# Kernel tuning notes

Measured on AMD Instinct MI355X. Metric: run time of the kernel, lower is better.

Reference implementation:

```python
import jax, jax.numpy as jnp
import numpy as np

B, N, C, W = 8, 2048, 256, 256

def setup_inputs() -> dict:
    key = jax.random.key(0)
    ks = jax.random.split(key, 8)
    x = jax.random.normal(ks[0], (B, N, C), dtype=jnp.float32)
    valid_len = jax.random.randint(ks[1], (B,), 0, N)
    # kaiming_normal_ on weights (fan_in = C), default bias init ~ U(-1/sqrt(C), 1/sqrt(C))
    std = np.sqrt(2.0 / C).astype(np.float32)
    bb = 1.0 / np.sqrt(C)
    Wq = jax.random.normal(ks[2], (W, C), dtype=jnp.float32) * std
    Wk = jax.random.normal(ks[3], (W, C), dtype=jnp.float32) * std
    Wv = jax.random.normal(ks[4], (W, C), dtype=jnp.float32) * std
    bq = jax.random.uniform(ks[5], (W,), dtype=jnp.float32, minval=-bb, maxval=bb)
    bk = jax.random.uniform(ks[6], (W,), dtype=jnp.float32, minval=-bb, maxval=bb)
    bv = jax.random.uniform(ks[7], (W,), dtype=jnp.float32, minval=-bb, maxval=bb)
    return {"x": x, "Wq": Wq, "bq": bq, "Wk": Wk, "bk": bk, "Wv": Wv, "bv": bv, "valid_len": valid_len}

def reference(x, Wq, bq, Wk, bk, Wv, bv, valid_len):
    # valid_len is unused in the original forward
    q = jax.nn.relu(jnp.einsum('bnc,wc->bnw', x, Wq) + bq)  # [B,N,W]
    k = jax.nn.relu(jnp.einsum('bnc,wc->bnw', x, Wk) + bk)
    v = jax.nn.relu(jnp.einsum('bnc,wc->bnw', x, Wv) + bv)
    scores = jnp.einsum('biw,bjw->bij', q, k) / jnp.sqrt(jnp.float32(k.shape[1]))  # [B,N,N]
    attn = jax.nn.softmax(scores, axis=1)  # NOTE: softmax over the QUERY axis (dim=1), as in source
    out = jnp.einsum('bij,bjw->biw', attn, v)
    return out + q
```

## Files before the change

kernel.cpp:

```cpp
#include <hip/hip_runtime.h>
#include <math.h>

#define Bb 8
#define Nn 2048
#define Cc 256
#define Ww 256
#define Mtot (Bb*Nn)

typedef __attribute__((ext_vector_type(8))) short bf16x8;
typedef __attribute__((ext_vector_type(4))) float f32x4;

__device__ __forceinline__ ushort bf16_rne(float f) {
    uint u = __float_as_uint(f);
    return (ushort)((u + 0x7FFFu + ((u >> 16) & 1u)) >> 16);
}
__device__ __forceinline__ float bf16_to_f32(ushort h) {
    return __uint_as_float(((uint)h) << 16);
}

__global__ __launch_bounds__(256) void prep_kernel(
    const float* __restrict__ x,
    const float* __restrict__ Wq, const float* __restrict__ Wk,
    const float* __restrict__ Wv,
    ushort* __restrict__ xh, ushort* __restrict__ xl,
    ushort* __restrict__ wqh, ushort* __restrict__ wql,
    ushort* __restrict__ wkh, ushort* __restrict__ wkl,
    ushort* __restrict__ wvh, ushort* __restrict__ wvl)
{
    const int tid = threadIdx.x;
    const float* src;
    ushort *dh, *dl;
    size_t off;
    if (blockIdx.x < 4096) {
        off = ((size_t)blockIdx.x * 256 + tid) * 4;
        src = x; dh = xh; dl = xl;
    } else {
        size_t s = ((size_t)(blockIdx.x - 4096) * 256 + tid) * 4;
        int which = (int)(s >> 16);
        off = s & 65535u;
        src = (which == 0) ? Wq : ((which == 1) ? Wk : Wv);
        dh  = (which == 0) ? wqh : ((which == 1) ? wkh : wvh);
        dl  = (which == 0) ? wql : ((which == 1) ? wkl : wvl);
    }
    float4 v = *(const float4*)(src + off);
    ushort4 h, l;
    h.x = bf16_rne(v.x); l.x = bf16_rne(v.x - bf16_to_f32(h.x));
    h.y = bf16_rne(v.y); l.y = bf16_rne(v.y - bf16_to_f32(h.y));
    h.z = bf16_rne(v.z); l.z = bf16_rne(v.z - bf16_to_f32(h.z));
    h.w = bf16_rne(v.w); l.w = bf16_rne(v.w - bf16_to_f32(h.w));
    *(ushort4*)(dh + off) = h;
    *(ushort4*)(dl + off) = l;
}

__global__ __launch_bounds__(256) void qkv_mfma_kernel(
    const ushort* __restrict__ xh, const ushort* __restrict__ xl,
    const ushort* __restrict__ wqh, const ushort* __restrict__ wql,
    const ushort* __restrict__ wkh, const ushort* __restrict__ wkl,
    const ushort* __restrict__ wvh, const ushort* __restrict__ wvl,
    const float* __restrict__ bq, const float* __restrict__ bk,
    const float* __restrict__ bv,
    float* __restrict__ v32,
    ushort* __restrict__ qhi, ushort* __restrict__ qlo,
    ushort* __restrict__ khi, ushort* __restrict__ klo)
{
    __shared__ ushort lah[4096], lal[4096], lbh[4096], lbl[4096];

    const int tid = threadIdx.x;
    const int m0 = blockIdx.x * 128;
    const int yy = blockIdx.y;
    const int which = yy >> 1;
    const int w0 = (yy & 1) * 128;

    const ushort* wh_ = (which == 0) ? wqh : ((which == 1) ? wkh : wvh);
    const ushort* wl_ = (which == 0) ? wql : ((which == 1) ? wkl : wvl);
    const float*  bm  = (which == 0) ? bq  : ((which == 1) ? bk  : bv);

    const ushort* ah_ = xh + (size_t)m0 * Cc;
    const ushort* al_ = xl + (size_t)m0 * Cc;
    const ushort* bh_ = wh_ + (size_t)w0 * Cc;
    const ushort* bl_ = wl_ + (size_t)w0 * Cc;

    const int wave = tid >> 6, lane = tid & 63;
    const int wy = wave >> 1, wx = wave & 1;
    const int lrow = lane & 15, lg = lane >> 4;

    f32x4 acc[4][4];
    #pragma unroll
    for (int a = 0; a < 4; ++a)
        #pragma unroll
        for (int c = 0; c < 4; ++c) acc[a][c] = (f32x4){0.f, 0.f, 0.f, 0.f};

    const int cg = tid & 3;
    const int cr0 = tid >> 2;

    for (int kc = 0; kc < Cc; kc += 32) {
        #pragma unroll
        for (int h = 0; h < 2; ++h) {
            int r = cr0 + h * 64;
            int gg = cg ^ ((r >> 1) & 3);
            int li = r * 32 + gg * 8;
            size_t go = (size_t)r * Cc + kc + cg * 8;
            *(bf16x8*)&lah[li] = *(const bf16x8*)(ah_ + go);
            *(bf16x8*)&lal[li] = *(const bf16x8*)(al_ + go);
            *(bf16x8*)&lbh[li] = *(const bf16x8*)(bh_ + go);
            *(bf16x8*)&lbl[li] = *(const bf16x8*)(bl_ + go);
        }
        __syncthreads();

        bf16x8 ah[4], al[4], bh[4], bl[4];
        #pragma unroll
        for (int t = 0; t < 4; ++t) {
            int ra = wy * 64 + t * 16 + lrow;
            int ia = ra * 32 + ((lg ^ ((ra >> 1) & 3)) * 8);
            ah[t] = *(const bf16x8*)&lah[ia];
            al[t] = *(const bf16x8*)&lal[ia];
            int rb = wx * 64 + t * 16 + lrow;
            int ib = rb * 32 + ((lg ^ ((rb >> 1) & 3)) * 8);
            bh[t] = *(const bf16x8*)&lbh[ib];
            bl[t] = *(const bf16x8*)&lbl[ib];
        }
        #pragma unroll
        for (int jt = 0; jt < 4; ++jt)
            #pragma unroll
            for (int it = 0; it < 4; ++it) {
                acc[jt][it] = __builtin_amdgcn_mfma_f32_16x16x32_bf16(ah[jt], bh[it], acc[jt][it], 0, 0, 0);
                acc[jt][it] = __builtin_amdgcn_mfma_f32_16x16x32_bf16(ah[jt], bl[it], acc[jt][it], 0, 0, 0);
                acc[jt][it] = __builtin_amdgcn_mfma_f32_16x16x32_bf16(al[jt], bh[it], acc[jt][it], 0, 0, 0);
            }
        __syncthreads();
    }

    ushort* hp = (which == 0) ? qhi : khi;
    ushort* lp = (which == 0) ? qlo : klo;
    #pragma unroll
    for (int it = 0; it < 4; ++it) {
        const int w = w0 + wx * 64 + it * 16 + lrow;
        const float bias = bm[w];
        #pragma unroll
        for (int jt = 0; jt < 4; ++jt) {
            const int mb = m0 + wy * 64 + jt * 16 + lg * 4;
            #pragma unroll
            for (int rg = 0; rg < 4; ++rg) {
                float val = fmaxf(acc[jt][it][rg] + bias, 0.f);
                size_t o = (size_t)(mb + rg) * Ww + w;
                if (which == 2) {
                    v32[o] = val;
                } else {
                    ushort h = bf16_rne(val);
                    hp[o] = h;
                    lp[o] = bf16_rne(val - bf16_to_f32(h));
                }
            }
        }
    }
}

__global__ __launch_bounds__(256) void scores_mfma_kernel(
    const ushort* __restrict__ qhi, const ushort* __restrict__ qlo,
    const ushort* __restrict__ khi, const ushort* __restrict__ klo,
    ushort* __restrict__ eh, float* __restrict__ dpart)
{
    __shared__ ushort lkh[4096], lkl[4096], lqh[4096], lql[4096];

    const int tid = threadIdx.x;
    const int i0 = blockIdx.x * 128;
    const int j0 = blockIdx.y * 128;
    const int b  = blockIdx.z;

    const ushort* kh = khi + ((size_t)b * Nn + j0) * Ww;
    const ushort* kl = klo + ((size_t)b * Nn + j0) * Ww;
    const ushort* qh = qhi + ((size_t)b * Nn + i0) * Ww;
    const ushort* ql = qlo + ((size_t)b * Nn + i0) * Ww;

    const int wave = tid >> 6, lane = tid & 63;
    const int wy = wave >> 1, wx = wave & 1;
    const int lrow = lane & 15, lg = lane >> 4;

    f32x4 acc[4][4];
    #pragma unroll
    for (int a = 0; a < 4; ++a)
        #pragma unroll
        for (int c = 0; c < 4; ++c) acc[a][c] = (f32x4){0.f, 0.f, 0.f, 0.f};

    const int cg = tid & 3;
    const int cr0 = tid >> 2;

    for (int kc = 0; kc < Ww; kc += 32) {
        #pragma unroll
        for (int h = 0; h < 2; ++h) {
            int r = cr0 + h * 64;
            int gg = cg ^ ((r >> 1) & 3);
            int li = r * 32 + gg * 8;
            size_t go = (size_t)r * Ww + kc + cg * 8;
            *(bf16x8*)&lkh[li] = *(const bf16x8*)(kh + go);
            *(bf16x8*)&lkl[li] = *(const bf16x8*)(kl + go);
            *(bf16x8*)&lqh[li] = *(const bf16x8*)(qh + go);
            *(bf16x8*)&lql[li] = *(const bf16x8*)(ql + go);
        }
        __syncthreads();

        bf16x8 ah[4], al[4], bh[4], bl[4];
        #pragma unroll
        for (int t = 0; t < 4; ++t) {
            int ra = wy * 64 + t * 16 + lrow;
            int ia = ra * 32 + ((lg ^ ((ra >> 1) & 3)) * 8);
            ah[t] = *(const bf16x8*)&lkh[ia];
            al[t] = *(const bf16x8*)&lkl[ia];
            int rb = wx * 64 + t * 16 + lrow;
            int ib = rb * 32 + ((lg ^ ((rb >> 1) & 3)) * 8);
            bh[t] = *(const bf16x8*)&lqh[ib];
            bl[t] = *(const bf16x8*)&lql[ib];
        }
        #pragma unroll
        for (int jt = 0; jt < 4; ++jt)
            #pragma unroll
            for (int it = 0; it < 4; ++it) {
                acc[jt][it] = __builtin_amdgcn_mfma_f32_16x16x32_bf16(ah[jt], bh[it], acc[jt][it], 0, 0, 0);
                acc[jt][it] = __builtin_amdgcn_mfma_f32_16x16x32_bf16(ah[jt], bl[it], acc[jt][it], 0, 0, 0);
                acc[jt][it] = __builtin_amdgcn_mfma_f32_16x16x32_bf16(al[jt], bh[it], acc[jt][it], 0, 0, 0);
            }
        __syncthreads();
    }

    const float scale = 0.02209708691207961f;
    ushort* ehb = eh + (size_t)b * Nn * Nn;
    float* dpb  = dpart + (size_t)b * Nn;

    float esum[4][4];
    #pragma unroll
    for (int jt = 0; jt < 4; ++jt)
        #pragma unroll
        for (int rg = 0; rg < 4; ++rg) esum[jt][rg] = 0.f;

    #pragma unroll
    for (int jt = 0; jt < 4; ++jt) {
        const int jb = j0 + wy * 64 + jt * 16 + lg * 4;
        #pragma unroll
        for (int it = 0; it < 4; ++it) {
            const int i = i0 + wx * 64 + it * 16 + lrow;
            ushort4 h4;
            #pragma unroll
            for (int rg = 0; rg < 4; ++rg) {
                float e = __expf(acc[jt][it][rg] * scale);
                ushort hh = bf16_rne(e);
                (&h4.x)[rg] = hh;
                esum[jt][rg] += bf16_to_f32(hh);
            }
            *(ushort4*)(ehb + (size_t)i * Nn + jb) = h4;
        }
    }
    #pragma unroll
    for (int jt = 0; jt < 4; ++jt)
        #pragma unroll
        for (int rg = 0; rg < 4; ++rg) {
            float v = esum[jt][rg];
            v += __shfl_xor(v, 1);
            v += __shfl_xor(v, 2);
            v += __shfl_xor(v, 4);
            v += __shfl_xor(v, 8);
            if (lrow == 0)
                atomicAdd(dpb + j0 + wy * 64 + jt * 16 + lg * 4 + rg, v);
        }
}

__global__ __launch_bounds__(256) void vt_kernel(
    const float* __restrict__ v32, const float* __restrict__ dpart,
    ushort* __restrict__ vthi, ushort* __restrict__ vtlo)
{
    __shared__ ushort Thi[64*66], Tlo[64*66];
    const int tid = threadIdx.x;
    const int j0 = blockIdx.x * 64;
    const int w0 = blockIdx.y * 64;
    const int b  = blockIdx.z;
    const float* vb = v32 + (size_t)b * Nn * Ww;
    const float* dpb = dpart + (size_t)b * Nn;

    #pragma unroll
    for (int r = 0; r < 4; ++r) {
        int j  = (tid >> 4) + r * 16;
        int wl = (tid & 15) * 4;
        float invd = 1.0f / dpb[j0 + j];
        float4 tv = *(const float4*)(vb + (size_t)(j0 + j) * Ww + w0 + wl);
        float f[4] = {tv.x * invd, tv.y * invd, tv.z * invd, tv.w * invd};
        #pragma unroll
        for (int c = 0; c < 4; ++c) {
            ushort h = bf16_rne(f[c]);
            Thi[(wl + c) * 66 + j] = h;
            Tlo[(wl + c) * 66 + j] = bf16_rne(f[c] - bf16_to_f32(h));
        }
    }
    __syncthreads();
    {
        int wl = tid >> 2, jc = (tid & 3) * 16;
        size_t go = ((size_t)b * Ww + w0 + wl) * Nn + j0 + jc;
        uint tH[8], tL[8];
        #pragma unroll
        for (int u = 0; u < 8; ++u) {
            tH[u] = *(const uint*)&Thi[wl * 66 + jc + u * 2];
            tL[u] = *(const uint*)&Tlo[wl * 66 + jc + u * 2];
        }
        #pragma unroll
        for (int u = 0; u < 2; ++u) {
            uint4 hh; hh.x = tH[u*4+0]; hh.y = tH[u*4+1]; hh.z = tH[u*4+2]; hh.w = tH[u*4+3];
            uint4 ll; ll.x = tL[u*4+0]; ll.y = tL[u*4+1]; ll.z = tL[u*4+2]; ll.w = tL[u*4+3];
            *(uint4*)(vthi + go + u * 8) = hh;
            *(uint4*)(vtlo + go + u * 8) = ll;
        }
    }
}

__global__ __launch_bounds__(256) void pv_mfma_kernel(
    const ushort* __restrict__ eh,
    const ushort* __restrict__ vthi, const ushort* __restrict__ vtlo,
    float* __restrict__ part)
{
    __shared__ alignas(16) ushort Ah[128*40];
    __shared__ alignas(16) ushort Bh[64*40], Bl[64*40];

    const int tid = threadIdx.x;
    const int i0 = blockIdx.x * 128;
    const int wt = blockIdx.y & 3, kz = blockIdx.y >> 2;
    const int w0 = wt * 64;
    const int b  = blockIdx.z;

    const ushort* ehb = eh + (size_t)b * Nn * Nn;
    const ushort* vhb = vthi + (size_t)b * Ww * Nn;
    const ushort* vlb = vtlo + (size_t)b * Ww * Nn;

    const int wave = tid >> 6, lane = tid & 63;
    const int wy = wave >> 1, wx = wave & 1;
    const int lr = lane & 15, lg = lane >> 4;

    f32x4 acc[4][2];
    #pragma unroll
    for (int a = 0; a < 4; ++a)
        #pragma unroll
        for (int c = 0; c < 2; ++c) acc[a][c] = (f32x4){0.f, 0.f, 0.f, 0.f};

    const bool isA = tid < 128;
    const int srow = isA ? tid : (tid & 63);
    const ushort* gsrc = isA ? ehb : ((tid & 64) ? vlb : vhb);
    const size_t goff0 = isA
        ? ((size_t)(i0 + srow) * Nn + (size_t)kz * 1024)
        : ((size_t)(w0 + srow) * Nn + (size_t)kz * 1024);
    ushort* ldst = isA ? &Ah[srow * 40] : ((tid & 64) ? &Bl[srow * 40] : &Bh[srow * 40]);

    bf16x8 r0 = *(const bf16x8*)(gsrc + goff0);
    bf16x8 r1 = *(const bf16x8*)(gsrc + goff0 + 8);
    bf16x8 r2 = *(const bf16x8*)(gsrc + goff0 + 16);
    bf16x8 r3 = *(const bf16x8*)(gsrc + goff0 + 24);

    for (int ks = 0; ks < 32; ++ks) {
        *(bf16x8*)(ldst)      = r0;
        *(bf16x8*)(ldst + 8)  = r1;
        *(bf16x8*)(ldst + 16) = r2;
        *(bf16x8*)(ldst + 24) = r3;
        __syncthreads();

        if (ks < 31) {
            const size_t go = goff0 + (ks + 1) * 32;
            r0 = *(const bf16x8*)(gsrc + go);
            r1 = *(const bf16x8*)(gsrc + go + 8);
            r2 = *(const bf16x8*)(gsrc + go + 16);
            r3 = *(const bf16x8*)(gsrc + go + 24);
        }

        bf16x8 af[4], bfh[2], bfl[2];
        #pragma unroll
        for (int t = 0; t < 4; ++t)
            af[t] = *(const bf16x8*)&Ah[(wy * 64 + t * 16 + lr) * 40 + lg * 8];
        #pragma unroll
        for (int t = 0; t < 2; ++t) {
            const int br = (wx * 32 + t * 16 + lr) * 40 + lg * 8;
            bfh[t] = *(const bf16x8*)&Bh[br];
            bfl[t] = *(const bf16x8*)&Bl[br];
        }
        #pragma unroll
        for (int ia = 0; ia < 4; ++ia)
            #pragma unroll
            for (int ib = 0; ib < 2; ++ib) {
                acc[ia][ib] = __builtin_amdgcn_mfma_f32_16x16x32_bf16(af[ia], bfh[ib], acc[ia][ib], 0, 0, 0);
                acc[ia][ib] = __builtin_amdgcn_mfma_f32_16x16x32_bf16(af[ia], bfl[ib], acc[ia][ib], 0, 0, 0);
            }
        __syncthreads();
    }

    float* pout = part + (size_t)kz * Mtot * Ww;
    #pragma unroll
    for (int ia = 0; ia < 4; ++ia) {
        const int ibase = i0 + wy * 64 + ia * 16 + lg * 4;
        #pragma unroll
        for (int ib = 0; ib < 2; ++ib) {
            const int w = w0 + wx * 32 + ib * 16 + lr;
            #pragma unroll
            for (int rg = 0; rg < 4; ++rg)
                pout[((size_t)(b * Nn + ibase + rg)) * Ww + w] = acc[ia][ib][rg];
        }
    }
}

__global__ __launch_bounds__(256) void qadd_kernel(
    const float* __restrict__ part,
    const ushort* __restrict__ qhi, const ushort* __restrict__ qlo,
    float* __restrict__ out)
{
    const size_t g4 = ((size_t)blockIdx.x * 256 + threadIdx.x) * 4;
    float4 p0 = *(const float4*)(part + g4);
    float4 p1 = *(const float4*)(part + (size_t)Mtot * Ww + g4);
    ushort4 h = *(const ushort4*)(qhi + g4);
    ushort4 l = *(const ushort4*)(qlo + g4);
    float4 o;
    o.x = p0.x + p1.x + bf16_to_f32(h.x) + bf16_to_f32(l.x);
    o.y = p0.y + p1.y + bf16_to_f32(h.y) + bf16_to_f32(l.y);
    o.z = p0.z + p1.z + bf16_to_f32(h.z) + bf16_to_f32(l.z);
    o.w = p0.w + p1.w + bf16_to_f32(h.w) + bf16_to_f32(l.w);
    *(float4*)(out + g4) = o;
}

extern "C" void kernel_launch(void* const* d_in, const int* in_sizes, int n_in,
                              void* d_out, int out_size, void* d_ws, size_t ws_size,
                              hipStream_t stream) {
    const float* x  = (const float*)d_in[0];
    const float* Wq = (const float*)d_in[1];
    const float* bq = (const float*)d_in[2];
    const float* Wk = (const float*)d_in[3];
    const float* bk = (const float*)d_in[4];
    const float* Wv = (const float*)d_in[5];
    const float* bv = (const float*)d_in[6];
    float* out = (float*)d_out;

    float*  v32 = (float*)d_ws;
    ushort* qhi = (ushort*)(v32 + (size_t)Mtot * Ww);
    ushort* qlo = qhi + (size_t)Mtot * Ww;
    ushort* khi = qlo + (size_t)Mtot * Ww;
    ushort* klo = khi + (size_t)Mtot * Ww;
    ushort* eh  = klo + (size_t)Mtot * Ww;
    float*  part = (float*)(eh + (size_t)Bb * Nn * Nn);
    float*  dpart = part + (size_t)2 * Mtot * Ww;
    ushort* xh  = (ushort*)(dpart + Bb * Nn);
    ushort* xl  = xh + (size_t)Mtot * Cc;
    ushort* wqh = xl + (size_t)Mtot * Cc;
    ushort* wql = wqh + Ww * Cc;
    ushort* wkh = wql + Ww * Cc;
    ushort* wkl = wkh + Ww * Cc;
    ushort* wvh = wkl + Ww * Cc;
    ushort* wvl = wvh + Ww * Cc;
    ushort* vthi = khi;
    ushort* vtlo = klo;

    hipMemsetAsync(dpart, 0, (size_t)Bb * Nn * sizeof(float), stream);
    prep_kernel<<<dim3(4288), 256, 0, stream>>>(x, Wq, Wk, Wv, xh, xl,
                                                wqh, wql, wkh, wkl, wvh, wvl);
    qkv_mfma_kernel<<<dim3(128, 6), 256, 0, stream>>>(xh, xl, wqh, wql, wkh, wkl,
                                                      wvh, wvl, bq, bk, bv,
                                                      v32, qhi, qlo, khi, klo);
    scores_mfma_kernel<<<dim3(16, 16, 8), 256, 0, stream>>>(qhi, qlo, khi, klo, eh, dpart);
    vt_kernel<<<dim3(32, 4, 8), 256, 0, stream>>>(v32, dpart, vthi, vtlo);
    pv_mfma_kernel<<<dim3(16, 8, 8), 256, 0, stream>>>(eh, vthi, vtlo, part);
    qadd_kernel<<<dim3(4096), 256, 0, stream>>>(part, qhi, qlo, out);
}
```

Measured before the change: 286.3 us.

## Register-prefetch next K tile in QKV/scores GEMMs and widen PV tile

The QKV and scores GEMM kernels now load the next K chunk from global memory into registers while the current chunk is consumed from LDS, which hides global latency behind the MFMA work. Separately, the PV kernel tile grows from 128x64 to 128x128 over W, so each block reuses the loaded attention tile across twice as many output columns. The grid halves in y to match. This reduces redundant reads of the large exp-score matrix at the cost of more registers, more LDS and fewer blocks.

```diff
diff --git a/kernel.cpp b/kernel.cpp
--- a/kernel.cpp
+++ b/kernel.cpp
@@ -93,19 +93,41 @@
     const int cg = tid & 3;
     const int cr0 = tid >> 2;
 
+    bf16x8 sah[2], sal[2], sbh[2], sbl[2];
+    #pragma unroll
+    for (int h = 0; h < 2; ++h) {
+        int r = cr0 + h * 64;
+        size_t go = (size_t)r * Cc + cg * 8;
+        sah[h] = *(const bf16x8*)(ah_ + go);
+        sal[h] = *(const bf16x8*)(al_ + go);
+        sbh[h] = *(const bf16x8*)(bh_ + go);
+        sbl[h] = *(const bf16x8*)(bl_ + go);
+    }
+
     for (int kc = 0; kc < Cc; kc += 32) {
         #pragma unroll
         for (int h = 0; h < 2; ++h) {
             int r = cr0 + h * 64;
             int gg = cg ^ ((r >> 1) & 3);
             int li = r * 32 + gg * 8;
-            size_t go = (size_t)r * Cc + kc + cg * 8;
-            *(bf16x8*)&lah[li] = *(const bf16x8*)(ah_ + go);
-            *(bf16x8*)&lal[li] = *(const bf16x8*)(al_ + go);
-            *(bf16x8*)&lbh[li] = *(const bf16x8*)(bh_ + go);
-            *(bf16x8*)&lbl[li] = *(const bf16x8*)(bl_ + go);
+            *(bf16x8*)&lah[li] = sah[h];
+            *(bf16x8*)&lal[li] = sal[h];
+            *(bf16x8*)&lbh[li] = sbh[h];
+            *(bf16x8*)&lbl[li] = sbl[h];
         }
         __syncthreads();
+
+        if (kc + 32 < Cc) {
+            #pragma unroll
+            for (int h = 0; h < 2; ++h) {
+                int r = cr0 + h * 64;
+                size_t go = (size_t)r * Cc + kc + 32 + cg * 8;
+                sah[h] = *(const bf16x8*)(ah_ + go);
+                sal[h] = *(const bf16x8*)(al_ + go);
+                sbh[h] = *(const bf16x8*)(bh_ + go);
+                sbl[h] = *(const bf16x8*)(bl_ + go);
+            }
+        }
 
         bf16x8 ah[4], al[4], bh[4], bl[4];
         #pragma unroll
@@ -185,19 +207,41 @@
     const int cg = tid & 3;
     const int cr0 = tid >> 2;
 
+    bf16x8 skh[2], skl[2], sqh[2], sql[2];
+    #pragma unroll
+    for (int h = 0; h < 2; ++h) {
+        int r = cr0 + h * 64;
+        size_t go = (size_t)r * Ww + cg * 8;
+        skh[h] = *(const bf16x8*)(kh + go);
+        skl[h] = *(const bf16x8*)(kl + go);
+        sqh[h] = *(const bf16x8*)(qh + go);
+        sql[h] = *(const bf16x8*)(ql + go);
+    }
+
     for (int kc = 0; kc < Ww; kc += 32) {
         #pragma unroll
         for (int h = 0; h < 2; ++h) {
             int r = cr0 + h * 64;
             int gg = cg ^ ((r >> 1) & 3);
             int li = r * 32 + gg * 8;
-            size_t go = (size_t)r * Ww + kc + cg * 8;
-            *(bf16x8*)&lkh[li] = *(const bf16x8*)(kh + go);
-            *(bf16x8*)&lkl[li] = *(const bf16x8*)(kl + go);
-            *(bf16x8*)&lqh[li] = *(const bf16x8*)(qh + go);
-            *(bf16x8*)&lql[li] = *(const bf16x8*)(ql + go);
+            *(bf16x8*)&lkh[li] = skh[h];
+            *(bf16x8*)&lkl[li] = skl[h];
+            *(bf16x8*)&lqh[li] = sqh[h];
+            *(bf16x8*)&lql[li] = sql[h];
         }
         __syncthreads();
+
+        if (kc + 32 < Ww) {
+            #pragma unroll
+            for (int h = 0; h < 2; ++h) {
+                int r = cr0 + h * 64;
+                size_t go = (size_t)r * Ww + kc + 32 + cg * 8;
+                skh[h] = *(const bf16x8*)(kh + go);
+                skl[h] = *(const bf16x8*)(kl + go);
+                sqh[h] = *(const bf16x8*)(qh + go);
+                sql[h] = *(const bf16x8*)(ql + go);
+            }
+        }
 
         bf16x8 ah[4], al[4], bh[4], bl[4];
         #pragma unroll
@@ -315,12 +359,12 @@
     float* __restrict__ part)
 {
     __shared__ alignas(16) ushort Ah[128*40];
-    __shared__ alignas(16) ushort Bh[64*40], Bl[64*40];
+    __shared__ alignas(16) ushort Bh[128*40], Bl[128*40];
 
     const int tid = threadIdx.x;
     const int i0 = blockIdx.x * 128;
-    const int wt = blockIdx.y & 3, kz = blockIdx.y >> 2;
-    const int w0 = wt * 64;
+    const int wt = blockIdx.y & 1, kz = blockIdx.y >> 1;
+    const int w0 = wt * 128;
     const int b  = blockIdx.z;
 
     const ushort* ehb = eh + (size_t)b * Nn * Nn;
@@ -331,54 +375,57 @@
     const int wy = wave >> 1, wx = wave & 1;
     const int lr = lane & 15, lg = lane >> 4;
 
-    f32x4 acc[4][2];
+    f32x4 acc[4][4];
     #pragma unroll
     for (int a = 0; a < 4; ++a)
         #pragma unroll
-        for (int c = 0; c < 2; ++c) acc[a][c] = (f32x4){0.f, 0.f, 0.f, 0.f};
-
-    const bool isA = tid < 128;
-    const int srow = isA ? tid : (tid & 63);
-    const ushort* gsrc = isA ? ehb : ((tid & 64) ? vlb : vhb);
-    const size_t goff0 = isA
-        ? ((size_t)(i0 + srow) * Nn + (size_t)kz * 1024)
-        : ((size_t)(w0 + srow) * Nn + (size_t)kz * 1024);
-    ushort* ldst = isA ? &Ah[srow * 40] : ((tid & 64) ? &Bl[srow * 40] : &Bh[srow * 40]);
-
-    bf16x8 r0 = *(const bf16x8*)(gsrc + goff0);
-    bf16x8 r1 = *(const bf16x8*)(gsrc + goff0 + 8);
-    bf16x8 r2 = *(const bf16x8*)(gsrc + goff0 + 16);
-    bf16x8 r3 = *(const bf16x8*)(gsrc + goff0 + 24);
+        for (int c = 0; c < 4; ++c) acc[a][c] = (f32x4){0.f, 0.f, 0.f, 0.f};
+
+    const int srow = tid >> 1;
+    const int sjc  = (tid & 1) * 16;
+    const size_t aoff0 = (size_t)(i0 + srow) * Nn + (size_t)kz * 1024 + sjc;
+    const size_t boff0 = (size_t)(w0 + srow) * Nn + (size_t)kz * 1024 + sjc;
+    const int lbase = srow * 40 + sjc;
+
+    bf16x8 ra0 = *(const bf16x8*)(ehb + aoff0);
+    bf16x8 ra1 = *(const bf16x8*)(ehb + aoff0 + 8);
+    bf16x8 rh0 = *(const bf16x8*)(vhb + boff0);
+    bf16x8 rh1 = *(const bf16x8*)(vhb + boff0 + 8);
+    bf16x8 rl0 = *(const bf16x8*)(vlb + boff0);
+    bf16x8 rl1 = *(const bf16x8*)(vlb + boff0 + 8);
 
     for (int ks = 0; ks < 32; ++ks) {
-        *(bf16x8*)(ldst)      = r0;
-        *(bf16x8*)(ldst + 8)  = r1;
-        *(bf16x8*)(ldst + 16) = r2;
-        *(bf16x8*)(ldst + 24) = r3;
+        *(bf16x8*)&Ah[lbase]     = ra0;
+        *(bf16x8*)&Ah[lbase + 8] = ra1;
+        *(bf16x8*)&Bh[lbase]     = rh0;
+        *(bf16x8*)&Bh[lbase + 8] = rh1;
+        *(bf16x8*)&Bl[lbase]     = rl0;
+        *(bf16x8*)&Bl[lbase + 8] = rl1;
         __syncthreads();
 
         if (ks < 31) {
-            const size_t go = goff0 + (ks + 1) * 32;
-            r0 = *(const bf16x8*)(gsrc + go);
-            r1 = *(const bf16x8*)(gsrc + go + 8);
-            r2 = *(const bf16x8*)(gsrc + go + 16);
-            r3 = *(const bf16x8*)(gsrc + go + 24);
-        }
-
-        bf16x8 af[4], bfh[2], bfl[2];
-        #pragma unroll
-        for (int t = 0; t < 4; ++t)
+            const size_t ao = aoff0 + (ks + 1) * 32;
+            const size_t bo = boff0 + (ks + 1) * 32;
+            ra0 = *(const bf16x8*)(ehb + ao);
+            ra1 = *(const bf16x8*)(ehb + ao + 8);
+            rh0 = *(const bf16x8*)(vhb + bo);
+            rh1 = *(const bf16x8*)(vhb + bo + 8);
+            rl0 = *(const bf16x8*)(vlb + bo);
+            rl1 = *(const bf16x8*)(vlb + bo + 8);
+        }
+
+        bf16x8 af[4], bfh[4], bfl[4];
+        #pragma unroll
+        for (int t = 0; t < 4; ++t) {
             af[t] = *(const bf16x8*)&Ah[(wy * 64 + t * 16 + lr) * 40 + lg * 8];
-        #pragma unroll
-        for (int t = 0; t < 2; ++t) {
-            const int br = (wx * 32 + t * 16 + lr) * 40 + lg * 8;
+            const int br = (wx * 64 + t * 16 + lr) * 40 + lg * 8;
             bfh[t] = *(const bf16x8*)&Bh[br];
             bfl[t] = *(const bf16x8*)&Bl[br];
         }
         #pragma unroll
         for (int ia = 0; ia < 4; ++ia)
             #pragma unroll
-            for (int ib = 0; ib < 2; ++ib) {
+            for (int ib = 0; ib < 4; ++ib) {
                 acc[ia][ib] = __builtin_amdgcn_mfma_f32_16x16x32_bf16(af[ia], bfh[ib], acc[ia][ib], 0, 0, 0);
                 acc[ia][ib] = __builtin_amdgcn_mfma_f32_16x16x32_bf16(af[ia], bfl[ib], acc[ia][ib], 0, 0, 0);
             }
@@ -390,8 +437,8 @@
     for (int ia = 0; ia < 4; ++ia) {
         const int ibase = i0 + wy * 64 + ia * 16 + lg * 4;
         #pragma unroll
-        for (int ib = 0; ib < 2; ++ib) {
-            const int w = w0 + wx * 32 + ib * 16 + lr;
+        for (int ib = 0; ib < 4; ++ib) {
+            const int w = w0 + wx * 64 + ib * 16 + lr;
             #pragma unroll
             for (int rg = 0; rg < 4; ++rg)
                 pout[((size_t)(b * Nn + ibase + rg)) * Ww + w] = acc[ia][ib][rg];
@@ -456,6 +503,6 @@
                                                       v32, qhi, qlo, khi, klo);
     scores_mfma_kernel<<<dim3(16, 16, 8), 256, 0, stream>>>(qhi, qlo, khi, klo, eh, dpart);
     vt_kernel<<<dim3(32, 4, 8), 256, 0, stream>>>(v32, dpart, vthi, vtlo);
-    pv_mfma_kernel<<<dim3(16, 8, 8), 256, 0, stream>>>(eh, vthi, vtlo, part);
+    pv_mfma_kernel<<<dim3(16, 4, 8), 256, 0, stream>>>(eh, vthi, vtlo, part);
     qadd_kernel<<<dim3(4096), 256, 0, stream>>>(part, qhi, qlo, out);
 }
```

After: 257.7 us. 1.11x faster.
